# Optimization experiments

Measured on AMD Instinct MI355X. Metric: run time of the kernel, lower is better.

Reference implementation:

```python
import jax, jax.numpy as jnp
import numpy as np

NUM_LAYERS = 6
D = 16           # physical_dim == bond_dim (required for multi-layer consistency)
B, S, FIN = 128, 2048, 128


def setup_inputs() -> dict:
    key = jax.random.key(0)
    k0, k1, k2, k3 = jax.random.split(key, 4)
    return {
        "sequence": jax.random.normal(k0, (B, S, FIN), jnp.float32),
        "W_emb": jax.random.normal(k1, (FIN, D), jnp.float32) * 0.05,
        "b_emb": jnp.zeros((D,), jnp.float32),
        "u": jax.random.normal(k2, (NUM_LAYERS, D, D, D, D), jnp.float32) * 0.1,
        "w": jax.random.normal(k3, (NUM_LAYERS, D, D, D), jnp.float32) * 0.1,
    }


def _ent_entropy(sA, sB):
    # sA: (B, pA, d), sB: (B, pB, d)
    corr = jnp.einsum('bik,bjk->bij', sA, sB)          # (B, pA, pB)
    s = jnp.linalg.svd(corr, compute_uv=False)          # (B, min(pA,pB))
    sn = s / (jnp.sum(s, axis=1, keepdims=True) + 1e-8)
    return -jnp.sum(sn * jnp.log(sn + 1e-8), axis=1)    # (B,)


def _phi_q(sites):
    # sites: (B, n, d), n >= 4 and even
    n = sites.shape[1]
    mid = n // 2
    S_int = _ent_entropy(sites[:, :mid], sites[:, mid:])
    A, Bp = sites[:, :mid], sites[:, mid:]
    S1 = _ent_entropy(A[:, :mid // 2], A[:, mid // 2:])
    S2 = _ent_entropy(Bp[:, :(n - mid) // 2], Bp[:, (n - mid) // 2:])
    return jnp.maximum(S_int - (S1 + S2), 0.0)


def _apply_layer(sites, u_l, w_l):
    # sites: (B, n, d) with n even. Disentangle adjacent pairs, then coarse-grain.
    b, n, d = sites.shape
    s = sites.reshape(b, n // 2, 2, d)
    # disentangler: einsum('ijkl,bi,bj->bkl') batched over pairs p
    comb = jnp.einsum('ijkl,bpi,bpj->bpkl', u_l, s[:, :, 0], s[:, :, 1])
    o1 = comb.mean(axis=3)   # mean over l -> (b, p, k)
    o2 = comb.mean(axis=2)   # mean over k -> (b, p, l)
    # isometry acts on consecutive disentangled pairs (o1_i, o2_i)
    return jnp.einsum('aij,bpi,bpj->bpa', w_l, o1, o2)  # (b, n//2, bond)


def reference(sequence, W_emb, b_emb, u, w):
    emb = sequence @ W_emb + b_emb                       # (B, S, D)
    norm = jnp.linalg.norm(emb, axis=-1, keepdims=True)
    sites = emb / jnp.maximum(norm, 1e-12)               # F.normalize(dim=-1)
    for l in range(NUM_LAYERS):
        sites = _apply_layer(sites, u[l], w[l])
    phi_q = _phi_q(sites)
    return sites, phi_q
```

## Files before the change

kernel.cpp:

```cpp
#include <hip/hip_runtime.h>
#include <hip/hip_bf16.h>
#include <math.h>

#define BATCH 128
#define SEQ   2048
#define FIN   128
#define DD    16
#define NLAYERS 6

#define BUFA_F  (BATCH*SEQ*DD)
#define BUFB_F  (BATCH*(SEQ/2)*DD)
#define COEF_OFF (BUFA_F + BUFB_F)
#define ENT_OFF  (COEF_OFF + NLAYERS*12288)

__global__ __launch_bounds__(256) void k_prep(const float* __restrict__ u,
                                              const float* __restrict__ w,
                                              float* __restrict__ coef) {
    int l  = blockIdx.x;
    int ij = threadIdx.x;
    const float* ub = u + (size_t)l*65536 + (size_t)ij*256;
    float a1[16], a2[16];
#pragma unroll
    for (int k = 0; k < 16; ++k) { a1[k] = 0.0f; a2[k] = 0.0f; }
#pragma unroll
    for (int k = 0; k < 16; ++k) {
#pragma unroll
        for (int z = 0; z < 16; ++z) {
            float v = ub[k*16 + z];
            a1[k] += v;
            a2[z] += v;
        }
    }
    float* ucb = coef + (size_t)l*12288 + ij*32;
#pragma unroll
    for (int k = 0; k < 16; ++k) {
        ucb[k]      = a1[k]*(1.0f/16.0f);
        ucb[16 + k] = a2[k]*(1.0f/16.0f);
    }
    const float* wb = w + (size_t)l*4096;
    float* wtb = coef + (size_t)l*12288 + 8192 + ij*16;
#pragma unroll
    for (int a = 0; a < 16; ++a) wtb[a] = wb[a*256 + ij];
}

__global__ __launch_bounds__(256) void k_embed(const float* __restrict__ seq,
                                               const float* __restrict__ W,
                                               const float* __restrict__ bias,
                                               float* __restrict__ out) {
    int t = threadIdx.x;
    size_t row = (size_t)blockIdx.x*256 + t;
    const float4* rp = (const float4*)seq + row*32;
    float acc[16];
#pragma unroll
    for (int d = 0; d < 16; ++d) acc[d] = bias[d];

#pragma unroll 8
    for (int kk = 0; kk < 32; ++kk) {
        float4 rv = rp[kk];
        const float* wr = W + kk*64;
#pragma unroll
        for (int d = 0; d < 16; ++d) acc[d] = fmaf(rv.x, wr[d],      acc[d]);
#pragma unroll
        for (int d = 0; d < 16; ++d) acc[d] = fmaf(rv.y, wr[16 + d], acc[d]);
#pragma unroll
        for (int d = 0; d < 16; ++d) acc[d] = fmaf(rv.z, wr[32 + d], acc[d]);
#pragma unroll
        for (int d = 0; d < 16; ++d) acc[d] = fmaf(rv.w, wr[48 + d], acc[d]);
    }
    float p = 0.0f;
#pragma unroll
    for (int d = 0; d < 16; ++d) p = fmaf(acc[d], acc[d], p);
    float inv = 1.0f / fmaxf(sqrtf(p), 1e-12f);
    float4* op = (float4*)(out + row*16);
    op[0] = make_float4(acc[0]*inv,  acc[1]*inv,  acc[2]*inv,  acc[3]*inv);
    op[1] = make_float4(acc[4]*inv,  acc[5]*inv,  acc[6]*inv,  acc[7]*inv);
    op[2] = make_float4(acc[8]*inv,  acc[9]*inv,  acc[10]*inv, acc[11]*inv);
    op[3] = make_float4(acc[12]*inv, acc[13]*inv, acc[14]*inv, acc[15]*inv);
}

__global__ __launch_bounds__(256) void k_layer(const float* __restrict__ in,
                                               float* __restrict__ outp,
                                               const float* __restrict__ coefl) {
    __shared__ float cbuf[8192];
    __shared__ float spl[64*36];
    int t = threadIdx.x;
    int og = t & 7, pg = t >> 3;
    int lane = t & 63, base = lane & ~7;

    const float4* wtf = (const float4*)(coefl + 8192);
    float4 wr0 = wtf[0*256 + t];
    float4 wr1 = wtf[1*256 + t];
    float4 wr2 = wtf[2*256 + t];
    float4 wr3 = wtf[3*256 + t];

    {
        const float4* ucf = (const float4*)coefl;
        float4* c4 = (float4*)cbuf;
#pragma unroll
        for (int it = 0; it < 8; ++it) c4[it*256 + t] = ucf[it*256 + t];
    }
    {
        const float4* ing = (const float4*)in + (size_t)blockIdx.x*512;
        float4 v0 = ing[t];
        float4 v1 = ing[t + 256];
        *(float4*)&spl[(t >> 3)*36 + (t & 7)*4]        = v0;
        *(float4*)&spl[((t >> 3) + 32)*36 + (t & 7)*4] = v1;
    }
    __syncthreads();

    float s1v[2][16];
#pragma unroll
    for (int pp = 0; pp < 2; ++pp) {
        int p = pg + pp*32;
#pragma unroll
        for (int g = 0; g < 4; ++g) {
            float4 v = *(const float4*)&spl[p*36 + 16 + g*4];
            s1v[pp][g*4+0]=v.x; s1v[pp][g*4+1]=v.y; s1v[pp][g*4+2]=v.z; s1v[pp][g*4+3]=v.w;
        }
    }

    float accv[2][4];
    accv[0][0]=0.f; accv[0][1]=0.f; accv[0][2]=0.f; accv[0][3]=0.f;
    accv[1][0]=0.f; accv[1][1]=0.f; accv[1][2]=0.f; accv[1][3]=0.f;

    for (int i = 0; i < 16; ++i) {
        float s0a = spl[pg*36 + i];
        float s0b = spl[(pg + 32)*36 + i];
        const float4* uc = (const float4*)&cbuf[i*512] + og;
#pragma unroll
        for (int j = 0; j < 16; ++j) {
            float4 cv = uc[j*8];
            float pa = s0a * s1v[0][j];
            float pb = s0b * s1v[1][j];
            accv[0][0] = fmaf(pa, cv.x, accv[0][0]);
            accv[0][1] = fmaf(pa, cv.y, accv[0][1]);
            accv[0][2] = fmaf(pa, cv.z, accv[0][2]);
            accv[0][3] = fmaf(pa, cv.w, accv[0][3]);
            accv[1][0] = fmaf(pb, cv.x, accv[1][0]);
            accv[1][1] = fmaf(pb, cv.y, accv[1][1]);
            accv[1][2] = fmaf(pb, cv.z, accv[1][2]);
            accv[1][3] = fmaf(pb, cv.w, accv[1][3]);
        }
    }
    __syncthreads();
    {
        float4* c4 = (float4*)cbuf;
        c4[0*256 + t] = wr0;
        c4[1*256 + t] = wr1;
        c4[2*256 + t] = wr2;
        c4[3*256 + t] = wr3;
    }
    __syncthreads();

    float o2f[2][16];
#pragma unroll
    for (int j = 0; j < 16; ++j) {
        int src = base + 4 + (j >> 2);
        o2f[0][j] = __shfl(accv[0][j & 3], src, 64);
        o2f[1][j] = __shfl(accv[1][j & 3], src, 64);
    }

    float r0a = 0.f, r1a = 0.f, r0b = 0.f, r1b = 0.f;
    for (int grp = 0; grp < 4; ++grp) {
#pragma unroll
        for (int c = 0; c < 4; ++c) {
            float o1a = __shfl(accv[0][c], base + grp, 64);
            float o1b = __shfl(accv[1][c], base + grp, 64);
            const float2* wrow = (const float2*)&cbuf[(grp*4 + c)*256] + og;
#pragma unroll
            for (int j = 0; j < 16; ++j) {
                float2 wv = wrow[j*8];
                float qa = o1a * o2f[0][j];
                float qb = o1b * o2f[1][j];
                r0a = fmaf(qa, wv.x, r0a);
                r1a = fmaf(qa, wv.y, r1a);
                r0b = fmaf(qb, wv.x, r0b);
                r1b = fmaf(qb, wv.y, r1b);
            }
        }
    }

    size_t gp = (size_t)blockIdx.x*64;
    *(float2*)&outp[(gp + pg)*16 + og*2]      = make_float2(r0a, r1a);
    *(float2*)&outp[(gp + pg + 32)*16 + og*2] = make_float2(r0b, r1b);
}

__device__ __forceinline__ void rot_cs(float al, float be, float ga, float& c, float& s) {
    float ze = (be - al) / (2.0f * ga);
    float tt = copysignf(1.0f, ze) / (fabsf(ze) + sqrtf(1.0f + ze*ze));
    c = 1.0f / sqrtf(1.0f + tt*tt);
    s = c * tt;
}

__global__ __launch_bounds__(64) void k_phi(const float* __restrict__ sites,
                                            float* __restrict__ ent) {
    __shared__ float S[512];
    __shared__ float C[256];
    __shared__ float sv[16];
    int bid = blockIdx.x;
    int role = bid >> 7;
    int b = bid & 127;
    int t = threadIdx.x;
    const float* sp = sites + (size_t)b*512;

    if (role == 0) {
        for (int x = t; x < 512; x += 64) S[x] = sp[x];
        __syncthreads();
        for (int e = t; e < 256; e += 64) {
            int i = e & 15, j = e >> 4;
            float a = 0.0f;
            for (int k = 0; k < 16; ++k) a = fmaf(S[i*16+k], S[(16+j)*16+k], a);
            C[j*16 + i] = a;
        }
        __syncthreads();
        for (int sw = 0; sw < 12; ++sw) {
            for (int r = 0; r < 15; ++r) {
                int pr = t >> 3, sub = t & 7;
                int p, q;
                if (pr == 0) { p = 15; q = r; }
                else { p = (r + pr) % 15; q = (r + 15 - pr) % 15; }
                float u0 = C[p*16 + 2*sub],   u1v = C[p*16 + 2*sub + 1];
                float v0 = C[q*16 + 2*sub],   v1v = C[q*16 + 2*sub + 1];
                float al = u0*u0 + u1v*u1v;
                float be = v0*v0 + v1v*v1v;
                float ga = u0*v0 + u1v*v1v;
                al += __shfl_xor(al,1); al += __shfl_xor(al,2); al += __shfl_xor(al,4);
                be += __shfl_xor(be,1); be += __shfl_xor(be,2); be += __shfl_xor(be,4);
                ga += __shfl_xor(ga,1); ga += __shfl_xor(ga,2); ga += __shfl_xor(ga,4);
                if (ga != 0.0f) {
                    float c, s; rot_cs(al, be, ga, c, s);
                    C[p*16 + 2*sub]     = fmaf(c, u0, -s*v0);
                    C[p*16 + 2*sub + 1] = fmaf(c, u1v, -s*v1v);
                    C[q*16 + 2*sub]     = fmaf(s, u0,  c*v0);
                    C[q*16 + 2*sub + 1] = fmaf(s, u1v, c*v1v);
                }
                __syncthreads();
            }
        }
        if (t < 16) {
            float s2 = 0.0f;
            for (int rr = 0; rr < 16; ++rr) { float v = C[t*16+rr]; s2 = fmaf(v, v, s2); }
            sv[t] = sqrtf(s2);
        }
        __syncthreads();
        if (t == 0) {
            float sum = 0.0f;
            for (int i2 = 0; i2 < 16; ++i2) sum += sv[i2];
            float den = sum + 1e-8f;
            float e2 = 0.0f;
            for (int i2 = 0; i2 < 16; ++i2) {
                float sn = sv[i2] / den;
                e2 -= sn * logf(sn + 1e-8f);
            }
            ent[b] = e2;
        }
    } else {
        int ro = (role == 1) ? 0 : 256;
        for (int x = t; x < 256; x += 64) S[x] = sp[ro + x];
        __syncthreads();
        if (t < 64) {
            int i = t & 7, j = t >> 3;
            float a = 0.0f;
            for (int k = 0; k < 16; ++k) a = fmaf(S[i*16+k], S[(8+j)*16+k], a);
            C[j*8 + i] = a;
        }
        __syncthreads();
        for (int sw = 0; sw < 12; ++sw) {
            for (int r = 0; r < 7; ++r) {
                if (t < 32) {
                    int pr = t >> 3, sub = t & 7;
                    int p, q;
                    if (pr == 0) { p = 7; q = r; }
                    else { p = (r + pr) % 7; q = (r + 7 - pr) % 7; }
                    float uu = C[p*8 + sub], vv = C[q*8 + sub];
                    float al = uu*uu, be = vv*vv, ga = uu*vv;
                    al += __shfl_xor(al,1); al += __shfl_xor(al,2); al += __shfl_xor(al,4);
                    be += __shfl_xor(be,1); be += __shfl_xor(be,2); be += __shfl_xor(be,4);
                    ga += __shfl_xor(ga,1); ga += __shfl_xor(ga,2); ga += __shfl_xor(ga,4);
                    if (ga != 0.0f) {
                        float c, s; rot_cs(al, be, ga, c, s);
                        C[p*8 + sub] = fmaf(c, uu, -s*vv);
                        C[q*8 + sub] = fmaf(s, uu,  c*vv);
                    }
                }
                __syncthreads();
            }
        }
        if (t < 8) {
            float s2 = 0.0f;
            for (int rr = 0; rr < 8; ++rr) { float v = C[t*8+rr]; s2 = fmaf(v, v, s2); }
            sv[t] = sqrtf(s2);
        }
        __syncthreads();
        if (t == 0) {
            float sum = 0.0f;
            for (int i2 = 0; i2 < 8; ++i2) sum += sv[i2];
            float den = sum + 1e-8f;
            float e2 = 0.0f;
            for (int i2 = 0; i2 < 8; ++i2) {
                float sn = sv[i2] / den;
                e2 -= sn * logf(sn + 1e-8f);
            }
            ent[role*128 + b] = e2;
        }
    }
}

__global__ __launch_bounds__(128) void k_phi2(const float* __restrict__ ent,
                                              float* __restrict__ phi) {
    int b = threadIdx.x;
    phi[b] = fmaxf(ent[b] - (ent[128 + b] + ent[256 + b]), 0.0f);
}

extern "C" void kernel_launch(void* const* d_in, const int* in_sizes, int n_in,
                              void* d_out, int out_size, void* d_ws, size_t ws_size,
                              hipStream_t stream) {
    const float* seq  = (const float*)d_in[0];
    const float* W    = (const float*)d_in[1];
    const float* bias = (const float*)d_in[2];
    const float* u    = (const float*)d_in[3];
    const float* w    = (const float*)d_in[4];
    float* out = (float*)d_out;
    float* ws  = (float*)d_ws;

    float* bufA  = ws;
    float* bufB  = ws + BUFA_F;
    float* coefw = ws + COEF_OFF;
    float* entb  = ws + ENT_OFF;

    k_prep <<<NLAYERS, 256, 0, stream>>>(u, w, coefw);
    k_embed<<<(BATCH*SEQ)/256, 256, 0, stream>>>(seq, W, bias, bufA);

    const float* lin[6]  = { bufA, bufB, bufA, bufB, bufA, bufB };
    float*       lout[6] = { bufB, bufA, bufB, bufA, bufB, out  };
    int npairs = BATCH * (SEQ/2);
    for (int l = 0; l < NLAYERS; ++l) {
        k_layer<<<npairs/64, 256, 0, stream>>>(lin[l], lout[l], coefw + (size_t)l*12288);
        npairs >>= 1;
    }
    k_phi <<<3*BATCH, 64, 0, stream>>>(out, entb);
    k_phi2<<<1, 128, 0, stream>>>(entb, out + BATCH*32*DD);
}
```

Measured before the change: 221.9 us.

## Fuse last three MERA layers into one shared-memory tail kernel and split embed rows

```diff
diff --git a/kernel.cpp b/kernel.cpp
--- a/kernel.cpp
+++ b/kernel.cpp
@@ -7,6 +7,7 @@
 #define FIN   128
 #define DD    16
 #define NLAYERS 6
+#define SST   20
 
 #define BUFA_F  (BATCH*SEQ*DD)
 #define BUFB_F  (BATCH*(SEQ/2)*DD)
@@ -47,35 +48,41 @@
                                                const float* __restrict__ W,
                                                const float* __restrict__ bias,
                                                float* __restrict__ out) {
+    __shared__ float wl[2048];
     int t = threadIdx.x;
-    size_t row = (size_t)blockIdx.x*256 + t;
+    for (int x = t; x < 2048; x += 256) wl[x] = W[x];
+    int q = t & 3;
+    size_t row = ((size_t)blockIdx.x*256 + t) >> 2;
+    float acc[4];
+    {
+        float4 bv = *(const float4*)(bias + q*4);
+        acc[0] = bv.x; acc[1] = bv.y; acc[2] = bv.z; acc[3] = bv.w;
+    }
+    __syncthreads();
+
     const float4* rp = (const float4*)seq + row*32;
-    float acc[16];
-#pragma unroll
-    for (int d = 0; d < 16; ++d) acc[d] = bias[d];
-
 #pragma unroll 8
     for (int kk = 0; kk < 32; ++kk) {
         float4 rv = rp[kk];
-        const float* wr = W + kk*64;
-#pragma unroll
-        for (int d = 0; d < 16; ++d) acc[d] = fmaf(rv.x, wr[d],      acc[d]);
-#pragma unroll
-        for (int d = 0; d < 16; ++d) acc[d] = fmaf(rv.y, wr[16 + d], acc[d]);
-#pragma unroll
-        for (int d = 0; d < 16; ++d) acc[d] = fmaf(rv.z, wr[32 + d], acc[d]);
-#pragma unroll
-        for (int d = 0; d < 16; ++d) acc[d] = fmaf(rv.w, wr[48 + d], acc[d]);
+        float rc[4] = { rv.x, rv.y, rv.z, rv.w };
+#pragma unroll
+        for (int c = 0; c < 4; ++c) {
+            float4 wv = *(const float4*)&wl[(kk*4 + c)*16 + q*4];
+            float s = rc[c];
+            acc[0] = fmaf(s, wv.x, acc[0]);
+            acc[1] = fmaf(s, wv.y, acc[1]);
+            acc[2] = fmaf(s, wv.z, acc[2]);
+            acc[3] = fmaf(s, wv.w, acc[3]);
+        }
     }
     float p = 0.0f;
 #pragma unroll
-    for (int d = 0; d < 16; ++d) p = fmaf(acc[d], acc[d], p);
+    for (int j = 0; j < 4; ++j) p = fmaf(acc[j], acc[j], p);
+    p += __shfl_xor(p, 1);
+    p += __shfl_xor(p, 2);
     float inv = 1.0f / fmaxf(sqrtf(p), 1e-12f);
-    float4* op = (float4*)(out + row*16);
-    op[0] = make_float4(acc[0]*inv,  acc[1]*inv,  acc[2]*inv,  acc[3]*inv);
-    op[1] = make_float4(acc[4]*inv,  acc[5]*inv,  acc[6]*inv,  acc[7]*inv);
-    op[2] = make_float4(acc[8]*inv,  acc[9]*inv,  acc[10]*inv, acc[11]*inv);
-    op[3] = make_float4(acc[12]*inv, acc[13]*inv, acc[14]*inv, acc[15]*inv);
+    *(float4*)(out + row*16 + q*4) = make_float4(acc[0]*inv, acc[1]*inv,
+                                                 acc[2]*inv, acc[3]*inv);
 }
 
 __global__ __launch_bounds__(256) void k_layer(const float* __restrict__ in,
@@ -183,6 +190,124 @@
     size_t gp = (size_t)blockIdx.x*64;
     *(float2*)&outp[(gp + pg)*16 + og*2]      = make_float2(r0a, r1a);
     *(float2*)&outp[(gp + pg + 32)*16 + og*2] = make_float2(r0b, r1b);
+}
+
+template<int P, bool LAST>
+__device__ __forceinline__ void layer_body(float* sL, const float* coef,
+                                           float* outp, int npg, int t, int bid) {
+    int og = t & 7, pg = t >> 3;
+    int lane = t & 63, base = lane & ~7;
+    bool act = pg < npg;
+
+    float accv[P][4];
+    float s1v[P][16];
+#pragma unroll
+    for (int pp = 0; pp < P; ++pp) { accv[pp][0]=0.f; accv[pp][1]=0.f; accv[pp][2]=0.f; accv[pp][3]=0.f; }
+
+    if (act) {
+#pragma unroll
+        for (int pp = 0; pp < P; ++pp) {
+            int r = 2*(pg + pp*32) + 1;
+#pragma unroll
+            for (int g = 0; g < 4; ++g) {
+                float4 v = *(const float4*)&sL[r*SST + g*4];
+                s1v[pp][g*4+0]=v.x; s1v[pp][g*4+1]=v.y; s1v[pp][g*4+2]=v.z; s1v[pp][g*4+3]=v.w;
+            }
+        }
+        for (int i = 0; i < 16; ++i) {
+            float s0[P];
+#pragma unroll
+            for (int pp = 0; pp < P; ++pp) s0[pp] = sL[(2*(pg + pp*32))*SST + i];
+            const float4* uc = (const float4*)&coef[i*512] + og;
+#pragma unroll
+            for (int j = 0; j < 16; ++j) {
+                float4 cv = uc[j*8];
+#pragma unroll
+                for (int pp = 0; pp < P; ++pp) {
+                    float p = s0[pp] * s1v[pp][j];
+                    accv[pp][0] = fmaf(p, cv.x, accv[pp][0]);
+                    accv[pp][1] = fmaf(p, cv.y, accv[pp][1]);
+                    accv[pp][2] = fmaf(p, cv.z, accv[pp][2]);
+                    accv[pp][3] = fmaf(p, cv.w, accv[pp][3]);
+                }
+            }
+        }
+    }
+    __syncthreads();
+
+    if (act) {
+        float o2f[P][16];
+#pragma unroll
+        for (int j = 0; j < 16; ++j) {
+            int src = base + 4 + (j >> 2);
+#pragma unroll
+            for (int pp = 0; pp < P; ++pp)
+                o2f[pp][j] = __shfl(accv[pp][j & 3], src, 64);
+        }
+        float r0[P], r1[P];
+#pragma unroll
+        for (int pp = 0; pp < P; ++pp) { r0[pp] = 0.f; r1[pp] = 0.f; }
+        for (int grp = 0; grp < 4; ++grp) {
+#pragma unroll
+            for (int c = 0; c < 4; ++c) {
+                float o1i[P];
+#pragma unroll
+                for (int pp = 0; pp < P; ++pp)
+                    o1i[pp] = __shfl(accv[pp][c], base + grp, 64);
+#pragma unroll
+                for (int j = 0; j < 16; ++j) {
+                    float2 wv = *(const float2*)&coef[8192 + ((grp*4+c)*16 + j)*16 + og*2];
+#pragma unroll
+                    for (int pp = 0; pp < P; ++pp) {
+                        float q = o1i[pp] * o2f[pp][j];
+                        r0[pp] = fmaf(q, wv.x, r0[pp]);
+                        r1[pp] = fmaf(q, wv.y, r1[pp]);
+                    }
+                }
+            }
+        }
+        if (LAST) {
+#pragma unroll
+            for (int pp = 0; pp < P; ++pp) {
+                int p = pg + pp*32;
+                *(float2*)&outp[((size_t)bid*32 + p)*16 + og*2] = make_float2(r0[pp], r1[pp]);
+            }
+        } else {
+#pragma unroll
+            for (int pp = 0; pp < P; ++pp) {
+                int p = pg + pp*32;
+                *(float2*)&sL[p*SST + og*2] = make_float2(r0[pp], r1[pp]);
+            }
+        }
+    }
+    __syncthreads();
+}
+
+__global__ __launch_bounds__(256) void k_tail(const float* __restrict__ in,
+                                              const float* __restrict__ coefg,
+                                              float* __restrict__ outp) {
+    __shared__ float coef[12288];
+    __shared__ float sL[256*SST];
+    int t = threadIdx.x, bid = blockIdx.x;
+
+    const float4* in4 = (const float4*)in + (size_t)bid*1024;
+#pragma unroll
+    for (int it = 0; it < 4; ++it) {
+        int f = it*256 + t;
+        *(float4*)&sL[(f >> 2)*SST + (f & 3)*4] = in4[f];
+    }
+#pragma unroll 1
+    for (int l = 0; l < 3; ++l) {
+        const float4* src = (const float4*)(coefg + (size_t)(3 + l)*12288);
+        __syncthreads();
+        for (int x = t; x < 3072; x += 256) ((float4*)coef)[x] = src[x];
+        __syncthreads();
+        switch (l) {
+            case 0: layer_body<4,false>(sL, coef, outp, 32, t, bid); break;
+            case 1: layer_body<2,false>(sL, coef, outp, 32, t, bid); break;
+            case 2: layer_body<1,true >(sL, coef, outp, 32, t, bid); break;
+        }
+    }
 }
 
 __device__ __forceinline__ void rot_cs(float al, float be, float ga, float& c, float& s) {
@@ -329,15 +454,13 @@
     float* entb  = ws + ENT_OFF;
 
     k_prep <<<NLAYERS, 256, 0, stream>>>(u, w, coefw);
-    k_embed<<<(BATCH*SEQ)/256, 256, 0, stream>>>(seq, W, bias, bufA);
-
-    const float* lin[6]  = { bufA, bufB, bufA, bufB, bufA, bufB };
-    float*       lout[6] = { bufB, bufA, bufB, bufA, bufB, out  };
-    int npairs = BATCH * (SEQ/2);
-    for (int l = 0; l < NLAYERS; ++l) {
-        k_layer<<<npairs/64, 256, 0, stream>>>(lin[l], lout[l], coefw + (size_t)l*12288);
-        npairs >>= 1;
-    }
+    k_embed<<<(BATCH*SEQ*4)/256, 256, 0, stream>>>(seq, W, bias, bufA);
+
+    k_layer<<<2048, 256, 0, stream>>>(bufA, bufB, coefw + 0*12288);
+    k_layer<<<1024, 256, 0, stream>>>(bufB, bufA, coefw + 1*12288);
+    k_layer<<< 512, 256, 0, stream>>>(bufA, bufB, coefw + 2*12288);
+    k_tail <<< 128, 256, 0, stream>>>(bufB, coefw, out);
+
     k_phi <<<3*BATCH, 64, 0, stream>>>(out, entb);
     k_phi2<<<1, 128, 0, stream>>>(entb, out + BATCH*32*DD);
 }
```

After: 232.3 us. 4.7% more time.
